# Performance work log

Hardware: AMD Instinct MI355X
Metric: run time of the kernel (lower is better)

## Reference

```python
import jax, jax.numpy as jnp
import numpy as np

TAU_MEM = 20.0
V_THRESH = 1.0
DECAY = float(np.exp(-1.0 / TAU_MEM))
SLOPE = 5.0  # fast-sigmoid surrogate slope


@jax.custom_vjp
def spike(x):
    # Heaviside spike with fast-sigmoid surrogate gradient
    return (x > 0).astype(x.dtype)

def _spike_fwd(x):
    return spike(x), x

def _spike_bwd(x, g):
    surr = 1.0 / (1.0 + SLOPE * jnp.abs(x)) ** 2
    return (g * surr,)

spike.defvjp(_spike_fwd, _spike_bwd)


def setup_inputs() -> dict:
    key = jax.random.key(0)
    k1, k2 = jax.random.split(key)
    B, T, n_in, n_out = 32, 1000, 1024, 512
    input_spikes_seq = (jax.random.uniform(k1, (B, T, n_in)) < 0.05).astype(jnp.float32)
    w_init_scale = 0.5
    W = jax.random.normal(k2, (n_out, n_in), dtype=jnp.float32) * (w_init_scale / np.sqrt(n_in))
    return {"input_spikes_seq": input_spikes_seq, "W": W}


def reference(input_spikes_seq, W):
    # input_spikes_seq: (B, T, n_in); W: (n_out, n_in) -> out: (B, T, n_out)
    B, T, _ = input_spikes_seq.shape
    n_out = W.shape[0]
    # Hoist the GEMM out of the time loop: (B,T,n_in) x (n_out,n_in) -> (B,T,n_out)
    I = jnp.einsum('bti,oi->bto', input_spikes_seq, W)
    I_t = jnp.transpose(I, (1, 0, 2))  # (T, B, n_out)

    def step(v, i_t):
        v = v * DECAY + i_t
        s = spike(v - V_THRESH)
        v = v * (1.0 - jax.lax.stop_gradient(s))  # reset, detached as in torch
        return v, s

    v0 = jnp.zeros((B, n_out), dtype=input_spikes_seq.dtype)
    _, out_t = jax.lax.scan(step, v0, I_t)  # out_t: (T, B, n_out)
    return jnp.transpose(out_t, (1, 0, 2))
```

## Files before the change

### kernel.cpp

```cpp
#include <hip/hip_runtime.h>


#define N_IN   1024
#define N_OUT  512
#define DECAY_F 0.95122942450071400910f
#define SCALE     17179869184.0
#define SCALE_INV 5.8207660913467407e-11f

typedef int  v4i  __attribute__((ext_vector_type(4)));
typedef int  v16i __attribute__((ext_vector_type(16)));

typedef __attribute__((address_space(1))) const void gv_t;
typedef __attribute__((address_space(3))) void lv_t;
__device__ __forceinline__ void gl16(const signed char* g, signed char* l) {
    __builtin_amdgcn_global_load_lds((gv_t*)g, (lv_t*)l, 16, 0, 0);
}

__global__ __launch_bounds__(256) void prep(const float* __restrict__ S,
                                            signed char* __restrict__ S8,
                                            const float* __restrict__ W,
                                            signed char* __restrict__ D8,
                                            int nS16blocks) {
    if ((int)blockIdx.x < nS16blocks) {
        const int g = blockIdx.x * 256 + threadIdx.x;
        const float4* p = reinterpret_cast<const float4*>(S) + (size_t)g * 4;
        union { signed char c[16]; int4 v; } u;
#pragma unroll
        for (int q = 0; q < 4; ++q) {
            const float4 v = p[q];
            u.c[q * 4 + 0] = (signed char)(v.x != 0.f);
            u.c[q * 4 + 1] = (signed char)(v.y != 0.f);
            u.c[q * 4 + 2] = (signed char)(v.z != 0.f);
            u.c[q * 4 + 3] = (signed char)(v.w != 0.f);
        }
        reinterpret_cast<int4*>(S8)[g] = u.v;
    } else {
        const int n  = blockIdx.x - nS16blocks;
        const int k0 = threadIdx.x * 4;
        const float4 wv = *reinterpret_cast<const float4*>(W + (size_t)n * N_IN + k0);
        const float ww[4] = {wv.x, wv.y, wv.z, wv.w};
        int pk[4] = {0, 0, 0, 0};
#pragma unroll
        for (int j = 0; j < 4; ++j) {
            long long wi = (long long)rint((double)ww[j] * SCALE);
            const int d0 = (int)((wi + 128) & 255) - 128; wi = (wi - d0) >> 8;
            const int d1 = (int)((wi + 128) & 255) - 128; wi = (wi - d1) >> 8;
            const int d2 = (int)((wi + 128) & 255) - 128; wi = (wi - d2) >> 8;
            const int d3 = (int)wi;
            pk[0] |= (d0 & 255) << (8 * j);
            pk[1] |= (d1 & 255) << (8 * j);
            pk[2] |= (d2 & 255) << (8 * j);
            pk[3] |= (d3 & 255) << (8 * j);
        }
#pragma unroll
        for (int d = 0; d < 4; ++d)
            *reinterpret_cast<int*>(D8 + (size_t)(d * N_OUT + n) * N_IN + k0) = pk[d];
    }
}

#define BM 256
#define BN 64
#define BK 64
#define TILEB (BM * BK)
#define BUFSZ (2 * TILEB)

__global__ __launch_bounds__(512, 2) void gemm_i8(
        const signed char* __restrict__ S8,
        const signed char* __restrict__ D8,
        float* __restrict__ I, int M) {
    extern __shared__ signed char lds[];

    const int tid  = threadIdx.x;
    const int lane = tid & 63;
    const int w    = tid >> 6;
    const int wwm  = w >> 1;
    const int wwn  = w & 1;

    const int nx  = M / BM;
    const int u   = (blockIdx.x & 7) * nx + (blockIdx.x >> 3);
    const int bm  = u >> 3;
    const int bn  = u & 7;
    const int m0 = bm * BM;
    const int n0 = bn * BN;

    const int lrow  = lane >> 2;
    const int sslot = (lane & 3) << 4;
    const int swzs  = ((lrow >> 1) & 3) << 4;
    const int scola = sslot ^ swzs;

    const signed char* aSrc0 = S8 + (size_t)(m0 + w * 16 + lrow) * N_IN + scola;
    const signed char* aSrc1 = aSrc0 + (size_t)128 * N_IN;
    const signed char* bSrc0 = D8 + (size_t)((w >> 2) * N_OUT + n0 + (w & 3) * 16 + lrow) * N_IN + scola;
    const signed char* bSrc1 = bSrc0 + (size_t)2 * N_OUT * N_IN;

    const int aDst0 = (w * 16) * 64;
    const int aDst1 = aDst0 + 128 * 64;
    const int bDst0 = TILEB + (w * 16) * 64;
    const int bDst1 = bDst0 + 128 * 64;

#define STAGE(bofs, kt) do {                                      \
        gl16(aSrc0 + (kt) * BK, lds + (bofs) + aDst0);            \
        gl16(aSrc1 + (kt) * BK, lds + (bofs) + aDst1);            \
        gl16(bSrc0 + (kt) * BK, lds + (bofs) + bDst0);            \
        gl16(bSrc1 + (kt) * BK, lds + (bofs) + bDst1);            \
    } while (0)

    v16i acc[2][4];
#pragma unroll
    for (int mf = 0; mf < 2; ++mf)
#pragma unroll
        for (int d = 0; d < 4; ++d)
#pragma unroll
            for (int i = 0; i < 16; ++i) acc[mf][d][i] = 0;

    const int fr = lane & 31;
    const int kh = (lane >> 5) * 16;
    const int swzr = ((fr >> 1) & 3) << 4;

#define COMPUTE(bofs)                                                             \
    _Pragma("unroll")                                                             \
    for (int ksub = 0; ksub < 2; ++ksub) {                                        \
        const int kbx = (ksub * 32 + kh) ^ swzr;                                  \
        v4i af0 = *reinterpret_cast<const v4i*>(lds + (bofs) + (wwm * 64 + fr) * 64 + kbx);      \
        v4i af1 = *reinterpret_cast<const v4i*>(lds + (bofs) + (wwm * 64 + 32 + fr) * 64 + kbx); \
        v4i bf[4];                                                                \
        _Pragma("unroll")                                                         \
        for (int d = 0; d < 4; ++d)                                               \
            bf[d] = *reinterpret_cast<const v4i*>(lds + (bofs) + TILEB + (d * 64 + wwn * 32 + fr) * 64 + kbx); \
        __builtin_amdgcn_s_setprio(1);                                            \
        _Pragma("unroll")                                                         \
        for (int d = 0; d < 4; ++d) {                                             \
            acc[0][d] = __builtin_amdgcn_mfma_i32_32x32x32_i8(af0, bf[d], acc[0][d], 0, 0, 0); \
            acc[1][d] = __builtin_amdgcn_mfma_i32_32x32x32_i8(af1, bf[d], acc[1][d], 0, 0, 0); \
        }                                                                         \
        __builtin_amdgcn_s_setprio(0);                                            \
    }

    STAGE(0, 0);
    STAGE(BUFSZ, 1);
    int bo0 = 0, bo1 = BUFSZ, bo2 = 2 * BUFSZ;

#pragma unroll 1
    for (int kt = 0; kt < 16; ++kt) {
        if (kt < 15) asm volatile("s_waitcnt vmcnt(4)" ::: "memory");
        else         asm volatile("s_waitcnt vmcnt(0)" ::: "memory");
        __syncthreads();
        if (kt + 2 <= 15) { STAGE(bo2, kt + 2); }
        COMPUTE(bo0);
        const int t = bo0; bo0 = bo1; bo1 = bo2; bo2 = t;
    }

    const int col = fr;
    const int rb_ = (lane >> 5) * 4;
#pragma unroll
    for (int mf = 0; mf < 2; ++mf) {
#pragma unroll
        for (int reg = 0; reg < 16; ++reg) {
            const int row = (reg & 3) + 8 * (reg >> 2) + rb_;
            const long long v =
                ((long long)acc[mf][3][reg] << 24) + ((long long)acc[mf][2][reg] << 16) +
                ((long long)acc[mf][1][reg] << 8) + (long long)acc[mf][0][reg];
            I[(size_t)(m0 + wwm * 64 + mf * 32 + row) * N_OUT + n0 + wwn * 32 + col] =
                (float)v * SCALE_INV;
        }
    }
}
#undef STAGE
#undef COMPUTE

#define UT 50
__global__ __launch_bounds__(64) void lif_scan3(float* __restrict__ IO, int T) {
    const int idx = blockIdx.x * 64 + threadIdx.x;
    const int b = idx >> 9, o = idx & (N_OUT - 1);
    float* p = IO + (size_t)b * T * N_OUT + o;
    float ca[UT], cb[UT];
    float v = 0.f;
#pragma unroll
    for (int j = 0; j < UT; ++j) ca[j] = p[(size_t)j * N_OUT];
#pragma unroll 1
    for (int t0 = 0; t0 < T; t0 += 2 * UT) {
        if (t0 + UT < T) {
#pragma unroll
            for (int j = 0; j < UT; ++j) cb[j] = p[(size_t)(t0 + UT + j) * N_OUT];
        }
#pragma unroll
        for (int j = 0; j < UT; ++j) {
            v = v * DECAY_F + ca[j];
            float s = (v > 1.0f) ? 1.0f : 0.f;
            v *= (1.f - s);
            ca[j] = s;
        }
#pragma unroll
        for (int j = 0; j < UT; ++j) p[(size_t)(t0 + j) * N_OUT] = ca[j];
        if (t0 + UT >= T) break;
        if (t0 + 2 * UT < T) {
#pragma unroll
            for (int j = 0; j < UT; ++j) ca[j] = p[(size_t)(t0 + 2 * UT + j) * N_OUT];
        }
#pragma unroll
        for (int j = 0; j < UT; ++j) {
            v = v * DECAY_F + cb[j];
            float s = (v > 1.0f) ? 1.0f : 0.f;
            v *= (1.f - s);
            cb[j] = s;
        }
#pragma unroll
        for (int j = 0; j < UT; ++j) p[(size_t)(t0 + UT + j) * N_OUT] = cb[j];
    }
}

__global__ __launch_bounds__(256) void transpose_w(const float* __restrict__ W,
                                                   float* __restrict__ WT) {
    __shared__ float t[32][33];
    const int k0 = blockIdx.x * 32;
    const int n0 = blockIdx.y * 32;
    const int lx = threadIdx.x & 31;
    const int ly = threadIdx.x >> 5;
#pragma unroll
    for (int r = ly; r < 32; r += 8)
        t[r][lx] = W[(size_t)(n0 + r) * N_IN + k0 + lx];
    __syncthreads();
#pragma unroll
    for (int r = ly; r < 32; r += 8)
        WT[(size_t)(k0 + r) * N_OUT + n0 + lx] = t[lx][r];
}

__global__ __launch_bounds__(256) void gather_rows(
        const float* __restrict__ S, const float* __restrict__ WT,
        float* __restrict__ I, int M) {
    const int wid  = blockIdx.x * 4 + (threadIdx.x >> 6);
    const int lane = threadIdx.x & 63;
    if (wid >= M) return;
    const float* srow = S + (size_t)wid * N_IN;
    float4 a0 = {0.f, 0.f, 0.f, 0.f};
    float4 a1 = {0.f, 0.f, 0.f, 0.f};
    float sv[16];
#pragma unroll
    for (int g = 0; g < 16; ++g) sv[g] = srow[g * 64 + lane];
#pragma unroll
    for (int g = 0; g < 16; ++g) {
        unsigned long long m = __ballot(sv[g] != 0.0f);
        while (m) {
            const int bb = __builtin_ctzll(m);
            m &= m - 1;
            const int k = g * 64 + bb;
            const float* wp = WT + (size_t)k * N_OUT + lane * 4;
            const float4 w0 = *reinterpret_cast<const float4*>(wp);
            const float4 w1 = *reinterpret_cast<const float4*>(wp + 256);
            a0.x += w0.x; a0.y += w0.y; a0.z += w0.z; a0.w += w0.w;
            a1.x += w1.x; a1.y += w1.y; a1.z += w1.z; a1.w += w1.w;
        }
    }
    float* op = I + (size_t)wid * N_OUT + lane * 4;
    *reinterpret_cast<float4*>(op) = a0;
    *reinterpret_cast<float4*>(op + 256) = a1;
}

extern "C" void kernel_launch(void* const* d_in, const int* in_sizes, int n_in,
                              void* d_out, int out_size, void* d_ws, size_t ws_size,
                              hipStream_t stream) {
    const float* S = (const float*)d_in[0];
    const float* W = (const float*)d_in[1];
    float* out = (float*)d_out;

    const int K = N_IN;
    const int M = in_sizes[0] / K;
    const int B = 32;
    const int T = M / B;

    const size_t s8_bytes = (size_t)M * N_IN;
    const size_t d8_bytes = (size_t)4 * N_OUT * N_IN;
    const size_t need = s8_bytes + d8_bytes;

    if (ws_size >= need && (M % BM) == 0 && ((M / BM) * (N_OUT / BN)) % 8 == 0) {
        signed char* S8 = (signed char*)d_ws;
        signed char* D8 = (signed char*)d_ws + s8_bytes;
        const int nS16blocks = (M * N_IN / 16) / 256;
        prep<<<nS16blocks + N_OUT, 256, 0, stream>>>(S, S8, W, D8, nS16blocks);
        const size_t lds_bytes = (size_t)3 * BUFSZ;
        gemm_i8<<<(M / BM) * (N_OUT / BN), 512, lds_bytes, stream>>>(S8, D8, out, M);
        lif_scan3<<<(B * N_OUT) / 64, 64, 0, stream>>>(out, T);
    } else if (ws_size >= (size_t)N_IN * N_OUT * sizeof(float) && (M % 4) == 0) {
        float* WT = (float*)d_ws;
        dim3 tg(N_IN / 32, N_OUT / 32);
        transpose_w<<<tg, 256, 0, stream>>>(W, WT);
        gather_rows<<<M / 4, 256, 0, stream>>>(S, WT, out, M);
        lif_scan3<<<(B * N_OUT) / 64, 64, 0, stream>>>(out, T);
    }
}
```

Measured before the change: 146.8 us.

## Interleave global-to-LDS staging with MFMA clusters in fully unrolled GEMM K-loop

Replaces the rolled triple-buffered K loop with a fully unrolled sequence of tile steps. Each step is split into four phases that interleave LDS fragment reads, one global_load_lds issue and a four-MFMA cluster, separated by explicit s_barrier and lgkmcnt waits. The aim is to spread memory traffic across the compute so loads and MFMAs overlap instead of issuing all staging at the top of each iteration. The cost is many more barriers per tile and larger code size, and the per-phase lockstep across waves could limit overlap.

```diff
diff --git a/kernel.cpp b/kernel.cpp
--- a/kernel.cpp
+++ b/kernel.cpp
@@ -64,6 +64,13 @@
 #define TILEB (BM * BK)
 #define BUFSZ (2 * TILEB)
 
+#define BARRIER __builtin_amdgcn_s_barrier()
+#define LGKM0 do { asm volatile("s_waitcnt lgkmcnt(0)" ::: "memory");             \
+                   __builtin_amdgcn_sched_barrier(0); } while (0)
+#define VMCNT_(n) asm volatile("s_waitcnt vmcnt(" #n ")" ::: "memory")
+#define LDV(off) (*reinterpret_cast<const v4i*>(lds + (off)))
+#define MFMA_I8 __builtin_amdgcn_mfma_i32_32x32x32_i8
+
 __global__ __launch_bounds__(512, 2) void gemm_i8(
         const signed char* __restrict__ S8,
         const signed char* __restrict__ D8,
@@ -98,13 +105,6 @@
     const int bDst0 = TILEB + (w * 16) * 64;
     const int bDst1 = bDst0 + 128 * 64;
 
-#define STAGE(bofs, kt) do {                                      \
-        gl16(aSrc0 + (kt) * BK, lds + (bofs) + aDst0);            \
-        gl16(aSrc1 + (kt) * BK, lds + (bofs) + aDst1);            \
-        gl16(bSrc0 + (kt) * BK, lds + (bofs) + bDst0);            \
-        gl16(bSrc1 + (kt) * BK, lds + (bofs) + bDst1);            \
-    } while (0)
-
     v16i acc[2][4];
 #pragma unroll
     for (int mf = 0; mf < 2; ++mf)
@@ -116,39 +116,101 @@
     const int fr = lane & 31;
     const int kh = (lane >> 5) * 16;
     const int swzr = ((fr >> 1) & 3) << 4;
-
-#define COMPUTE(bofs)                                                             \
-    _Pragma("unroll")                                                             \
-    for (int ksub = 0; ksub < 2; ++ksub) {                                        \
-        const int kbx = (ksub * 32 + kh) ^ swzr;                                  \
-        v4i af0 = *reinterpret_cast<const v4i*>(lds + (bofs) + (wwm * 64 + fr) * 64 + kbx);      \
-        v4i af1 = *reinterpret_cast<const v4i*>(lds + (bofs) + (wwm * 64 + 32 + fr) * 64 + kbx); \
-        v4i bf[4];                                                                \
-        _Pragma("unroll")                                                         \
-        for (int d = 0; d < 4; ++d)                                               \
-            bf[d] = *reinterpret_cast<const v4i*>(lds + (bofs) + TILEB + (d * 64 + wwn * 32 + fr) * 64 + kbx); \
+    const int kx0 = kh ^ swzr;
+    const int kx1 = (32 + kh) ^ swzr;
+    const int ra0 = (wwm * 64 + fr) * 64;
+    const int ra1 = (wwm * 64 + 32 + fr) * 64;
+    const int rb0 = (0 * 64 + wwn * 32 + fr) * 64;
+    const int rb1 = (1 * 64 + wwn * 32 + fr) * 64;
+    const int rb2 = (2 * 64 + wwn * 32 + fr) * 64;
+    const int rb3 = (3 * 64 + wwn * 32 + fr) * 64;
+
+#define TILE_STEP(CUR, STG, KT, DOSTAGE, VML)                                     \
+    {                                                                             \
+        const int base = (CUR) * BUFSZ;                                           \
+        v4i af0, af1, bf0, bf1, bf2, bf3;                                         \
+                                                                     \
+        af0 = LDV(base + ra0 + kx0);                                              \
+        af1 = LDV(base + ra1 + kx0);                                              \
+        bf0 = LDV(base + TILEB + rb0 + kx0);                                      \
+        bf1 = LDV(base + TILEB + rb1 + kx0);                                      \
+        if (DOSTAGE) gl16(aSrc0 + (KT + 2) * BK, lds + (STG) * BUFSZ + aDst0);    \
+        BARRIER; LGKM0;                                                           \
         __builtin_amdgcn_s_setprio(1);                                            \
-        _Pragma("unroll")                                                         \
-        for (int d = 0; d < 4; ++d) {                                             \
-            acc[0][d] = __builtin_amdgcn_mfma_i32_32x32x32_i8(af0, bf[d], acc[0][d], 0, 0, 0); \
-            acc[1][d] = __builtin_amdgcn_mfma_i32_32x32x32_i8(af1, bf[d], acc[1][d], 0, 0, 0); \
-        }                                                                         \
+        acc[0][0] = MFMA_I8(af0, bf0, acc[0][0], 0, 0, 0);                        \
+        acc[1][0] = MFMA_I8(af1, bf0, acc[1][0], 0, 0, 0);                        \
+        acc[0][1] = MFMA_I8(af0, bf1, acc[0][1], 0, 0, 0);                        \
+        acc[1][1] = MFMA_I8(af1, bf1, acc[1][1], 0, 0, 0);                        \
         __builtin_amdgcn_s_setprio(0);                                            \
-    }
-
-    STAGE(0, 0);
-    STAGE(BUFSZ, 1);
-    int bo0 = 0, bo1 = BUFSZ, bo2 = 2 * BUFSZ;
-
-#pragma unroll 1
-    for (int kt = 0; kt < 16; ++kt) {
-        if (kt < 15) asm volatile("s_waitcnt vmcnt(4)" ::: "memory");
-        else         asm volatile("s_waitcnt vmcnt(0)" ::: "memory");
-        __syncthreads();
-        if (kt + 2 <= 15) { STAGE(bo2, kt + 2); }
-        COMPUTE(bo0);
-        const int t = bo0; bo0 = bo1; bo1 = bo2; bo2 = t;
-    }
+        BARRIER;                                                                  \
+                                                                     \
+        bf2 = LDV(base + TILEB + rb2 + kx0);                                      \
+        bf3 = LDV(base + TILEB + rb3 + kx0);                                      \
+        if (DOSTAGE) gl16(aSrc1 + (KT + 2) * BK, lds + (STG) * BUFSZ + aDst1);    \
+        BARRIER; LGKM0;                                                           \
+        __builtin_amdgcn_s_setprio(1);                                            \
+        acc[0][2] = MFMA_I8(af0, bf2, acc[0][2], 0, 0, 0);                        \
+        acc[1][2] = MFMA_I8(af1, bf2, acc[1][2], 0, 0, 0);                        \
+        acc[0][3] = MFMA_I8(af0, bf3, acc[0][3], 0, 0, 0);                        \
+        acc[1][3] = MFMA_I8(af1, bf3, acc[1][3], 0, 0, 0);                        \
+        __builtin_amdgcn_s_setprio(0);                                            \
+        BARRIER;                                                                  \
+                                                                     \
+        af0 = LDV(base + ra0 + kx1);                                              \
+        af1 = LDV(base + ra1 + kx1);                                              \
+        bf0 = LDV(base + TILEB + rb0 + kx1);                                      \
+        bf1 = LDV(base + TILEB + rb1 + kx1);                                      \
+        if (DOSTAGE) gl16(bSrc0 + (KT + 2) * BK, lds + (STG) * BUFSZ + bDst0);    \
+        BARRIER; LGKM0;                                                           \
+        __builtin_amdgcn_s_setprio(1);                                            \
+        acc[0][0] = MFMA_I8(af0, bf0, acc[0][0], 0, 0, 0);                        \
+        acc[1][0] = MFMA_I8(af1, bf0, acc[1][0], 0, 0, 0);                        \
+        acc[0][1] = MFMA_I8(af0, bf1, acc[0][1], 0, 0, 0);                        \
+        acc[1][1] = MFMA_I8(af1, bf1, acc[1][1], 0, 0, 0);                        \
+        __builtin_amdgcn_s_setprio(0);                                            \
+        BARRIER;                                                                  \
+                                                                     \
+        bf2 = LDV(base + TILEB + rb2 + kx1);                                      \
+        bf3 = LDV(base + TILEB + rb3 + kx1);                                      \
+        if (DOSTAGE) gl16(bSrc1 + (KT + 2) * BK, lds + (STG) * BUFSZ + bDst1);    \
+        BARRIER; LGKM0;                                                           \
+        __builtin_amdgcn_s_setprio(1);                                            \
+        acc[0][2] = MFMA_I8(af0, bf2, acc[0][2], 0, 0, 0);                        \
+        acc[1][2] = MFMA_I8(af1, bf2, acc[1][2], 0, 0, 0);                        \
+        acc[0][3] = MFMA_I8(af0, bf3, acc[0][3], 0, 0, 0);                        \
+        acc[1][3] = MFMA_I8(af1, bf3, acc[1][3], 0, 0, 0);                        \
+        __builtin_amdgcn_s_setprio(0);                                            \
+        VMCNT_(VML);                                                              \
+        BARRIER;                                                                  \
+    }
+
+    gl16(aSrc0, lds + aDst0);
+    gl16(aSrc1, lds + aDst1);
+    gl16(bSrc0, lds + bDst0);
+    gl16(bSrc1, lds + bDst1);
+    gl16(aSrc0 + BK, lds + BUFSZ + aDst0);
+    gl16(aSrc1 + BK, lds + BUFSZ + aDst1);
+    gl16(bSrc0 + BK, lds + BUFSZ + bDst0);
+    gl16(bSrc1 + BK, lds + BUFSZ + bDst1);
+    VMCNT_(4);
+    BARRIER;
+
+    TILE_STEP(0, 2, 0,  1, 4)
+    TILE_STEP(1, 0, 1,  1, 4)
+    TILE_STEP(2, 1, 2,  1, 4)
+    TILE_STEP(0, 2, 3,  1, 4)
+    TILE_STEP(1, 0, 4,  1, 4)
+    TILE_STEP(2, 1, 5,  1, 4)
+    TILE_STEP(0, 2, 6,  1, 4)
+    TILE_STEP(1, 0, 7,  1, 4)
+    TILE_STEP(2, 1, 8,  1, 4)
+    TILE_STEP(0, 2, 9,  1, 4)
+    TILE_STEP(1, 0, 10, 1, 4)
+    TILE_STEP(2, 1, 11, 1, 4)
+    TILE_STEP(0, 2, 12, 1, 4)
+    TILE_STEP(1, 0, 13, 1, 4)
+    TILE_STEP(2, 1, 14, 0, 0)
+    TILE_STEP(0, 0, 15, 0, 0)
 
     const int col = fr;
     const int rb_ = (lane >> 5) * 4;
@@ -165,8 +227,7 @@
         }
     }
 }
-#undef STAGE
-#undef COMPUTE
+#undef TILE_STEP
 
 #define UT 50
 __global__ __launch_bounds__(64) void lif_scan3(float* __restrict__ IO, int T) {
```

After: 141.5 us. -3.6%, faster.
